# Kernel optimization log

Hardware: AMD Instinct MI355X
Metric: run time of the kernel (lower is better)

## Reference

```python
import jax, jax.numpy as jnp
import numpy as np

NUM_CLASS = 3
LIMIT = 576.0 * 576.0   # from __init__ default limit=576*576
EPS = 1e-5              # normalize_with_limit eps
COS_EPS = 1e-8          # cosine_similarity eps
BIG = 1e9               # 'infinity' for EDT init (>> max possible squared dist)


def _edt(mask):
    """Exact Euclidean distance transform of a binary [H,W] mask.
    For nonzero pixels: distance to nearest zero pixel (scipy semantics).
    Separable squared EDT via brute-force min-plus 1D transforms."""
    H, W = mask.shape
    f = jnp.where(mask > 0, jnp.float32(BIG), jnp.float32(0.0))  # [H,W] sq dists
    jw = jnp.arange(W, dtype=jnp.float32)
    r2w = (jw[:, None] - jw[None, :]) ** 2  # [W,W] (j-k)^2
    jh = jnp.arange(H, dtype=jnp.float32)
    r2h = (jh[:, None] - jh[None, :]) ** 2  # [H,H]
    # pass along width: d[i,j] = min_k f[i,k] + (j-k)^2
    d = jnp.min(f[:, None, :] + r2w[None, :, :], axis=-1)        # [H,W]
    # pass along height: d[i,j] = min_k d[k,j] + (i-k)^2
    d = jnp.min(d.T[:, None, :] + r2h[None, :, :], axis=-1).T    # [H,W]
    return jnp.sqrt(d)


def _norm_limit(x):
    m = jnp.minimum(jnp.max(x), jnp.float32(LIMIT))
    return x / (m + jnp.float32(EPS))


def _dw(mask):
    return _norm_limit(_edt(mask))


def setup_inputs() -> dict:
    key = jax.random.key(0)
    k1, k2 = jax.random.split(key)
    B, C, H, W = 4, NUM_CLASS, 256, 256
    pred = jax.random.normal(k1, (B, C, H, W), dtype=jnp.float32)
    lab = jax.random.randint(k2, (B, H, W), 0, C, dtype=jnp.int32)
    return {"pred": pred, "lab": lab}


def reference(pred, lab):
    B, C, H, W = pred.shape
    pred_lbl = jnp.argmax(pred, axis=1)              # [B,H,W]
    lab = lab.reshape(pred_lbl.shape)

    lab_oh = jax.nn.one_hot(lab, C, dtype=jnp.float32)        # [B,H,W,C]
    pred_oh = jax.nn.one_hot(pred_lbl, C, dtype=jnp.float32)  # [B,H,W,C]
    lab_oh_c = jnp.moveaxis(lab_oh, -1, 1)           # [B,C,H,W] == getBAV masks
    pred_oh_c = jnp.moveaxis(pred_oh, -1, 1)

    # per-class distance weights (normalized EDT) -- sequential map keeps memory low
    lab_dw = jax.lax.map(_dw, lab_oh_c.reshape(B * C, H, W)).reshape(B, C, H, W)
    pred_dw = jax.lax.map(_dw, pred_oh_c.reshape(B * C, H, W)).reshape(B, C, H, W)

    # feat = [sum_c dw ; one_hot] -> [B, 1+C, H, W]
    lab_feat = jnp.concatenate([jnp.sum(lab_dw, axis=1, keepdims=True), lab_oh_c], axis=1)
    pred_feat = jnp.concatenate([jnp.sum(pred_dw, axis=1, keepdims=True), pred_oh_c], axis=1)

    # cosine similarity per pixel over the (1+C)=4 channel dim
    dot = jnp.sum(pred_feat * lab_feat, axis=1)                # [B,H,W]
    na = jnp.sqrt(jnp.sum(pred_feat * pred_feat, axis=1))
    nb = jnp.sqrt(jnp.sum(lab_feat * lab_feat, axis=1))
    sim = dot / (jnp.maximum(na, COS_EPS) * jnp.maximum(nb, COS_EPS))

    loss_b = 1.0 - jnp.mean(sim.reshape(B, -1), axis=1)        # [B]
    has_fg = jnp.sum((lab > 0).astype(jnp.int32), axis=(1, 2)) > 0
    loss = jnp.sum(jnp.where(has_fg, loss_b, 0.0)) / B
    return jnp.nan_to_num(loss, nan=0.0, posinf=1.0, neginf=0.0)
```

## Files before the change

kernel.cpp:

```cpp
#include <hip/hip_runtime.h>
#include <hip/hip_bf16.h>

#define HH 256
#define WW 256
#define BB 4
#define CC 3
#define HW 65536
#define NM 24
#define BIGF 1e9f
#define LIMITF 331776.0f
#define EPSF 1e-5f

__global__ __launch_bounds__(256) void k_rowpass(const float* __restrict__ pred,
                                                 const int* __restrict__ lab,
                                                 float* __restrict__ dbuf) {
    int blk = blockIdx.x;
    int b = blk >> 8;
    int i = blk & 255;
    int j = threadIdx.x;

    int lv = lab[(b << 16) + (i << 8) + j];
    const float* pb = pred + (((size_t)(b * 3)) << 16) + (i << 8) + j;
    float p0 = pb[0];
    float p1 = pb[(size_t)1 << 16];
    float p2 = pb[(size_t)2 << 16];
    int am = 0; float v = p0;
    if (p1 > v) { am = 1; v = p1; }
    if (p2 > v) { am = 2; }

    __shared__ unsigned long long zm[6][4];
    int w = threadIdx.x >> 6;
    #pragma unroll
    for (int c = 0; c < 3; ++c) {
        unsigned long long zl = __ballot(lv != c);
        unsigned long long zp = __ballot(am != c);
        if ((threadIdx.x & 63) == 0) { zm[c][w] = zl; zm[3 + c][w] = zp; }
    }
    __syncthreads();

    #pragma unroll
    for (int t = 0; t < 6; ++t) {
        int bestd = 512;
        #pragma unroll
        for (int w2 = 0; w2 < 4; ++w2) {
            unsigned long long z = zm[t][w2];
            int base = w2 << 6;
            int rel = j - base;
            unsigned long long mle;
            if (rel >= 63)      mle = ~0ULL;
            else if (rel < 0)   mle = 0ULL;
            else                mle = (2ULL << rel) - 1ULL;
            unsigned long long zl = z & mle;
            if (zl) {
                int p = base + 63 - __clzll(zl);
                int d = j - p;
                if (d < bestd) bestd = d;
            }
            unsigned long long zr = z & ~mle;
            if (zr) {
                int p = base + __ffsll(zr) - 1;
                int d = p - j;
                if (d < bestd) bestd = d;
            }
        }
        float d1 = (bestd >= 512) ? BIGF : (float)(bestd * bestd);
        int c = (t < 3) ? t : (t - 3);
        int m = ((t < 3) ? 0 : 12) + b * 3 + c;
        dbuf[(((size_t)m) << 16) + (i << 8) + j] = d1;
    }
}

__global__ __launch_bounds__(256) void k_colpass(float* __restrict__ dbuf,
                                                 float* __restrict__ blkmax) {
    int blk = blockIdx.x;
    int m = blk >> 5;
    int j0 = (blk & 31) << 3;
    __shared__ float tile[256 * 9];
    float* base = dbuf + (((size_t)m) << 16);

    #pragma unroll
    for (int it = 0; it < 2; ++it) {
        int f = (it << 8) + threadIdx.x;
        int row = f >> 1, half = f & 1;
        float4 v = *(const float4*)(base + (row << 8) + j0 + (half << 2));
        int lb = row * 9 + (half << 2);
        tile[lb + 0] = v.x; tile[lb + 1] = v.y;
        tile[lb + 2] = v.z; tile[lb + 3] = v.w;
    }
    __syncthreads();

    int jj = threadIdx.x & 7;
    int ib = threadIdx.x >> 3;
    float lmax = 0.0f;

    #pragma unroll
    for (int r = 0; r < 8; ++r) {
        int i = ib + (r << 5);
        float di = tile[i * 9 + jj];
        float acc = di;
        int R = (int)sqrtf(di) + 1;
        if (R > 255) R = 255;
        int k0 = i - R; if (k0 < 0) k0 = 0;
        int k1 = i + R; if (k1 > 255) k1 = 255;
        for (int k = k0; k <= k1; ++k) {
            float dk = (float)(k - i);
            acc = fminf(acc, fmaf(dk, dk, tile[k * 9 + jj]));
        }
        base[(i << 8) + j0 + jj] = acc;
        lmax = fmaxf(lmax, acc);
    }

    #pragma unroll
    for (int off = 32; off; off >>= 1)
        lmax = fmaxf(lmax, __shfl_down(lmax, off, 64));
    __shared__ float wmax[4];
    if ((threadIdx.x & 63) == 0) wmax[threadIdx.x >> 6] = lmax;
    __syncthreads();
    if (threadIdx.x == 0)
        blkmax[blk] = fmaxf(fmaxf(wmax[0], wmax[1]), fmaxf(wmax[2], wmax[3]));
}

__global__ __launch_bounds__(256) void k_final(const float* __restrict__ pred,
                                               const int* __restrict__ lab,
                                               const float* __restrict__ dbuf,
                                               const float* __restrict__ blkmax,
                                               float* __restrict__ psum,
                                               int* __restrict__ pfg) {
    __shared__ float inv[NM];
    if (threadIdx.x < NM) {
        const float* bm = blkmax + (threadIdx.x << 5);
        float v = 0.0f;
        #pragma unroll
        for (int s = 0; s < 32; ++s) v = fmaxf(v, bm[s]);
        inv[threadIdx.x] = 1.0f / (fminf(sqrtf(v), LIMITF) + EPSF);
    }
    __syncthreads();

    int b = blockIdx.x >> 8;
    int pix = ((blockIdx.x & 255) << 8) + threadIdx.x;

    int lv = lab[(b << 16) + pix];
    const float* pb = pred + (((size_t)(b * 3)) << 16) + pix;
    float p0 = pb[0];
    float p1 = pb[(size_t)1 << 16];
    float p2 = pb[(size_t)2 << 16];
    int am = 0; float v = p0;
    if (p1 > v) { am = 1; v = p1; }
    if (p2 > v) { am = 2; }

    float slab = 0.0f, spred = 0.0f;
    #pragma unroll
    for (int c = 0; c < 3; ++c) {
        int ml = b * 3 + c;
        float dl = dbuf[(((size_t)ml) << 16) + pix];
        slab += sqrtf(dl) * inv[ml];
        float dp = dbuf[(((size_t)(ml + 12)) << 16) + pix];
        spred += sqrtf(dp) * inv[ml + 12];
    }

    float dot = spred * slab + ((am == lv) ? 1.0f : 0.0f);
    float na = sqrtf(spred * spred + 1.0f);
    float nb = sqrtf(slab * slab + 1.0f);
    float sim = dot / (fmaxf(na, 1e-8f) * fmaxf(nb, 1e-8f));

    unsigned long long fg = __ballot(lv > 0);

    #pragma unroll
    for (int off = 32; off; off >>= 1)
        sim += __shfl_down(sim, off, 64);
    __shared__ float wsum[4];
    __shared__ int wfg[4];
    if ((threadIdx.x & 63) == 0) {
        wsum[threadIdx.x >> 6] = sim;
        wfg[threadIdx.x >> 6] = (fg != 0ULL) ? 1 : 0;
    }
    __syncthreads();
    if (threadIdx.x == 0) {
        psum[blockIdx.x] = wsum[0] + wsum[1] + wsum[2] + wsum[3];
        pfg[blockIdx.x] = wfg[0] | wfg[1] | wfg[2] | wfg[3];
    }
}

__global__ __launch_bounds__(256) void k_finalize(const float* __restrict__ psum,
                                                  const int* __restrict__ pfg,
                                                  float* __restrict__ out) {
    int t = threadIdx.x;
    int b = t >> 6, l = t & 63;
    int base = (b << 8) + l;
    float s = psum[base] + psum[base + 64] + psum[base + 128] + psum[base + 192];
    int f = pfg[base] | pfg[base + 64] | pfg[base + 128] | pfg[base + 192];
    #pragma unroll
    for (int off = 32; off; off >>= 1) {
        s += __shfl_down(s, off, 64);
        f |= __shfl_down(f, off, 64);
    }
    __shared__ float bsum[4];
    __shared__ int bfg[4];
    if (l == 0) { bsum[b] = s; bfg[b] = f; }
    __syncthreads();
    if (t == 0) {
        float loss = 0.0f;
        for (int bb = 0; bb < BB; ++bb) {
            float lb = 1.0f - bsum[bb] * (1.0f / (float)HW);
            if (bfg[bb]) loss += lb;
        }
        loss *= (1.0f / (float)BB);
        if (isnan(loss)) loss = 0.0f;
        else if (isinf(loss)) loss = (loss > 0.0f) ? 1.0f : 0.0f;
        out[0] = loss;
    }
}

extern "C" void kernel_launch(void* const* d_in, const int* in_sizes, int n_in,
                              void* d_out, int out_size, void* d_ws, size_t ws_size,
                              hipStream_t stream) {
    const float* pred = (const float*)d_in[0];
    const int*   lab  = (const int*)d_in[1];

    char* wsb = (char*)d_ws;
    float* dbuf   = (float*)wsb;
    size_t off    = (size_t)NM * HW * sizeof(float);
    float* blkmax = (float*)(wsb + off);          off += 768 * sizeof(float);
    float* psum   = (float*)(wsb + off);          off += 1024 * sizeof(float);
    int*   pfg    = (int*)  (wsb + off);

    k_rowpass <<<BB * HH,  256, 0, stream>>>(pred, lab, dbuf);
    k_colpass <<<NM * 32,  256, 0, stream>>>(dbuf, blkmax);
    k_final   <<<BB * 256, 256, 0, stream>>>(pred, lab, dbuf, blkmax, psum, pfg);
    k_finalize<<<1,        256, 0, stream>>>(psum, pfg, (float*)d_out);
}
```

Baseline: 84.34 us.

## Cache label/argmax codes as bytes and make column pass wave-uniform

The row pass now writes a one-byte code per pixel holding the label and the argmax class. The final kernel reads this code instead of reloading pred (three floats) and lab, which cuts global reads. The column pass replaces per-pixel variable-length min-plus loops with one wave-wide maximum radius and a uniform offset loop over 8 rows held in registers. This removes divergence, but every lane now does as many iterations as the worst pixel in its wave, so some work is redundant.

```diff
diff --git a/kernel.cpp b/kernel.cpp
--- a/kernel.cpp
+++ b/kernel.cpp
@@ -11,9 +11,11 @@
 #define LIMITF 331776.0f
 #define EPSF 1e-5f
 
+
 __global__ __launch_bounds__(256) void k_rowpass(const float* __restrict__ pred,
                                                  const int* __restrict__ lab,
-                                                 float* __restrict__ dbuf) {
+                                                 float* __restrict__ dbuf,
+                                                 unsigned char* __restrict__ codes) {
     int blk = blockIdx.x;
     int b = blk >> 8;
     int i = blk & 255;
@@ -27,6 +29,8 @@
     int am = 0; float v = p0;
     if (p1 > v) { am = 1; v = p1; }
     if (p2 > v) { am = 2; }
+
+    codes[(b << 16) + (i << 8) + j] = (unsigned char)(lv | (am << 2));
 
     __shared__ unsigned long long zm[6][4];
     int w = threadIdx.x >> 6;
@@ -82,32 +86,47 @@
     for (int it = 0; it < 2; ++it) {
         int f = (it << 8) + threadIdx.x;
         int row = f >> 1, half = f & 1;
-        float4 v = *(const float4*)(base + (row << 8) + j0 + (half << 2));
+        float4 v4 = *(const float4*)(base + (row << 8) + j0 + (half << 2));
         int lb = row * 9 + (half << 2);
-        tile[lb + 0] = v.x; tile[lb + 1] = v.y;
-        tile[lb + 2] = v.z; tile[lb + 3] = v.w;
+        tile[lb + 0] = v4.x; tile[lb + 1] = v4.y;
+        tile[lb + 2] = v4.z; tile[lb + 3] = v4.w;
     }
     __syncthreads();
 
     int jj = threadIdx.x & 7;
     int ib = threadIdx.x >> 3;
+
+    float di[8], acc[8];
+    float dmax = 0.0f;
+    #pragma unroll
+    for (int r = 0; r < 8; ++r) {
+        di[r] = tile[(ib + (r << 5)) * 9 + jj];
+        acc[r] = di[r];
+        dmax = fmaxf(dmax, di[r]);
+    }
+    #pragma unroll
+    for (int off = 32; off; off >>= 1)
+        dmax = fmaxf(dmax, __shfl_xor(dmax, off, 64));
+    int Rmax = (int)sqrtf(dmax) + 1;
+    if (Rmax > 255) Rmax = 255;
+
+    for (int o = -Rmax; o <= Rmax; ++o) {
+        #pragma unroll
+        for (int r = 0; r < 8; ++r) {
+            int i = ib + (r << 5);
+            int k = i + o;
+            k = (k < 0) ? 0 : ((k > 255) ? 255 : k);
+            float dk = (float)(k - i);
+            acc[r] = fminf(acc[r], fmaf(dk, dk, tile[k * 9 + jj]));
+        }
+    }
+
     float lmax = 0.0f;
-
     #pragma unroll
     for (int r = 0; r < 8; ++r) {
         int i = ib + (r << 5);
-        float di = tile[i * 9 + jj];
-        float acc = di;
-        int R = (int)sqrtf(di) + 1;
-        if (R > 255) R = 255;
-        int k0 = i - R; if (k0 < 0) k0 = 0;
-        int k1 = i + R; if (k1 > 255) k1 = 255;
-        for (int k = k0; k <= k1; ++k) {
-            float dk = (float)(k - i);
-            acc = fminf(acc, fmaf(dk, dk, tile[k * 9 + jj]));
-        }
-        base[(i << 8) + j0 + jj] = acc;
-        lmax = fmaxf(lmax, acc);
+        base[(i << 8) + j0 + jj] = acc[r];
+        lmax = fmaxf(lmax, acc[r]);
     }
 
     #pragma unroll
@@ -120,8 +139,7 @@
         blkmax[blk] = fmaxf(fmaxf(wmax[0], wmax[1]), fmaxf(wmax[2], wmax[3]));
 }
 
-__global__ __launch_bounds__(256) void k_final(const float* __restrict__ pred,
-                                               const int* __restrict__ lab,
+__global__ __launch_bounds__(256) void k_final(const unsigned char* __restrict__ codes,
                                                const float* __restrict__ dbuf,
                                                const float* __restrict__ blkmax,
                                                float* __restrict__ psum,
@@ -139,14 +157,9 @@
     int b = blockIdx.x >> 8;
     int pix = ((blockIdx.x & 255) << 8) + threadIdx.x;
 
-    int lv = lab[(b << 16) + pix];
-    const float* pb = pred + (((size_t)(b * 3)) << 16) + pix;
-    float p0 = pb[0];
-    float p1 = pb[(size_t)1 << 16];
-    float p2 = pb[(size_t)2 << 16];
-    int am = 0; float v = p0;
-    if (p1 > v) { am = 1; v = p1; }
-    if (p2 > v) { am = 2; }
+    int code = codes[(b << 16) + pix];
+    int lv = code & 3;
+    int am = code >> 2;
 
     float slab = 0.0f, spred = 0.0f;
     #pragma unroll
@@ -222,10 +235,11 @@
     size_t off    = (size_t)NM * HW * sizeof(float);
     float* blkmax = (float*)(wsb + off);          off += 768 * sizeof(float);
     float* psum   = (float*)(wsb + off);          off += 1024 * sizeof(float);
-    int*   pfg    = (int*)  (wsb + off);
-
-    k_rowpass <<<BB * HH,  256, 0, stream>>>(pred, lab, dbuf);
+    int*   pfg    = (int*)  (wsb + off);          off += 1024 * sizeof(int);
+    unsigned char* codes = (unsigned char*)(wsb + off);
+
+    k_rowpass <<<BB * HH,  256, 0, stream>>>(pred, lab, dbuf, codes);
     k_colpass <<<NM * 32,  256, 0, stream>>>(dbuf, blkmax);
-    k_final   <<<BB * 256, 256, 0, stream>>>(pred, lab, dbuf, blkmax, psum, pfg);
+    k_final   <<<BB * 256, 256, 0, stream>>>(codes, dbuf, blkmax, psum, pfg);
     k_finalize<<<1,        256, 0, stream>>>(psum, pfg, (float*)d_out);
 }
```

Measured after the change: 81.90 us. -2.9%, faster.
